# Optimization experiments

Hardware: AMD Instinct MI355X
Metric: run time of the kernel (lower is better)

Reference implementation:

```python
import jax, jax.numpy as jnp
import numpy as np
from jax import lax

B, N, M = 512, 200, 20          # batch, jobs, machines
H1, ME, DI, H2, JD, AH = 128, 32, 128, 256, 256, 256


def setup_inputs() -> dict:
    key = jax.random.key(0)
    ks = jax.random.split(key, 18)
    g = lambda i, s, sc=1.0: jax.random.normal(ks[i], s, jnp.float32) * sc
    return {
        "encoded_jobs": g(0, (B, N, JD)),
        "all_job_processing_times": jax.random.uniform(ks[1], (B, N, M, 2), jnp.float32),
        "num_machines_scalar": jnp.full((B,), float(M), jnp.float32),
        # step1: RNN over machines (input dim 2) + machine-count embedding + FC -> di
        "rnn1_Wih": g(2, (H1, 2), 0.1),
        "rnn1_Whh": g(3, (H1, H1), 0.1),
        "rnn1_b": g(4, (H1,), 0.1),
        "m_w": g(5, (ME,), 0.1),
        "m_b": g(6, (ME,), 0.1),
        "fc_W": g(7, (DI, H1 + ME), 0.1),
        "fc_b": g(8, (DI,), 0.1),
        # step2: single-step RNN cell, initial hidden d0*
        "d0_h": g(9, (1, 1, H2), 0.1),
        "rnn2_Wih": g(10, (H2, DI), 0.1),
        "rnn2_Whh": g(11, (H2, H2), 0.1),
        "rnn2_b": g(12, (H2,), 0.1),
        # additive (Bahdanau) pointer attention
        "att_W1": g(13, (AH, JD), 0.1),
        "att_b1": g(14, (AH,), 0.1),
        "att_W2": g(15, (AH, H2), 0.1),
        "att_b2": g(16, (AH,), 0.1),
        "att_v": g(17, (AH,), 0.1),
    }


def _decode(encoded_jobs, pt, nm, rnn1_Wih, rnn1_Whh, rnn1_b, m_w, m_b,
            fc_W, fc_b, d0_h, rnn2_Wih, rnn2_Whh, rnn2_b,
            att_W1, att_b1, att_W2, att_b2, att_v):
    Bsz, Nn, _ = encoded_jobs.shape
    Mn = pt.shape[2]
    H1d = rnn1_Whh.shape[0]
    H2d = rnn2_Whh.shape[0]
    batch_idx = jnp.arange(Bsz)
    # precompute the job-side attention projection once (same math as per-step)
    pre_att = jnp.einsum('bnd,ad->bna', encoded_jobs, att_W1) + att_b1   # [B,N,AH]
    m_emb = nm[:, None] * m_w[None, :] + m_b                             # [B,ME]

    def step1(P_prev):  # P_prev: [B, M, 2] -> di [B, DI]
        def cell(h, x):
            return jnp.tanh(x @ rnn1_Wih.T + h @ rnn1_Whh.T + rnn1_b), None
        hT, _ = lax.scan(cell, jnp.zeros((Bsz, H1d), P_prev.dtype),
                         jnp.swapaxes(P_prev, 0, 1))
        return jnp.concatenate([hT, m_emb], axis=-1) @ fc_W.T + fc_b

    def decode_step(carry, skey):
        P_prev, h2, avail = carry
        di = step1(P_prev)
        h2n = jnp.tanh(di @ rnn2_Wih.T + h2 @ rnn2_Whh.T + rnn2_b)      # [B,H2]
        q = h2n @ att_W2.T + att_b2                                      # [B,AH]
        scores = jnp.tanh(pre_att + q[:, None, :]) @ att_v               # [B,N]
        masked = jnp.where(avail, scores, -1e9)
        probs = jax.nn.softmax(masked, axis=-1)
        logp = jnp.log(probs + 1e-9)
        chosen = jax.random.categorical(skey, masked)                    # multinomial(probs)
        P_next = pt[batch_idx, chosen]                                   # [B,M,2]
        avail = avail.at[batch_idx, chosen].set(False)
        return (P_next, h2n, avail), (chosen, logp)

    carry0 = (jnp.zeros((Bsz, Mn, 2), encoded_jobs.dtype),
              jnp.broadcast_to(d0_h[0], (Bsz, H2d)),
              jnp.ones((Bsz, Nn), dtype=bool))
    keys = jax.random.split(jax.random.key(42), Nn)  # max_decode_len = N
    _, (idx, logps) = lax.scan(decode_step, carry0, keys)
    return jnp.swapaxes(idx, 0, 1), jnp.swapaxes(logps, 0, 1)  # [B,T], [B,T,N]


def reference(encoded_jobs, all_job_processing_times, num_machines_scalar,
              rnn1_Wih, rnn1_Whh, rnn1_b, m_w, m_b, fc_W, fc_b, d0_h,
              rnn2_Wih, rnn2_Whh, rnn2_b, att_W1, att_b1, att_W2, att_b2, att_v):
    idx, logps = _decode(encoded_jobs, all_job_processing_times, num_machines_scalar,
                         rnn1_Wih, rnn1_Whh, rnn1_b, m_w, m_b, fc_W, fc_b, d0_h,
                         rnn2_Wih, rnn2_Whh, rnn2_b, att_W1, att_b1, att_W2, att_b2, att_v)
    return idx, logps, encoded_jobs
```

## Files before the change

### kernel.cpp

```cpp
#include <hip/hip_runtime.h>
#include <hip/hip_bf16.h>
#include <stdint.h>

#define BB 512
#define NN 200
#define TT 200
#define MM 20
#define H1N 128
#define MEN 32
#define DIN 128
#define H2N 256
#define JDN 256
#define AHN 256

#define PRE_REG 20
#define PRE_LDSB 32

typedef float f4v __attribute__((ext_vector_type(4)));

__device__ __forceinline__ void tf2x32(uint32_t k0, uint32_t k1,
                                       uint32_t x0, uint32_t x1,
                                       uint32_t& o0, uint32_t& o1) {
  uint32_t ks2 = k0 ^ k1 ^ 0x1BD11BDAu;
  x0 += k0; x1 += k1;
#define TF_RND(R) { x0 += x1; x1 = (x1 << (R)) | (x1 >> (32 - (R))); x1 ^= x0; }
  TF_RND(13) TF_RND(15) TF_RND(26) TF_RND(6)   x0 += k1;  x1 += ks2 + 1u;
  TF_RND(17) TF_RND(29) TF_RND(16) TF_RND(24)  x0 += ks2; x1 += k0 + 2u;
  TF_RND(13) TF_RND(15) TF_RND(26) TF_RND(6)   x0 += k0;  x1 += k1 + 3u;
  TF_RND(17) TF_RND(29) TF_RND(16) TF_RND(24)  x0 += k1;  x1 += ks2 + 4u;
  TF_RND(13) TF_RND(15) TF_RND(26) TF_RND(6)   x0 += ks2; x1 += k0 + 5u;
#undef TF_RND
  o0 = x0; o1 = x1;
}

__device__ __forceinline__ float ftanh(float x) {
  float e = __builtin_amdgcn_exp2f(x * 2.8853900817779268f);
  float d = e + 1.0f;
  float r = __builtin_amdgcn_rcpf(d);
  r = r * (2.0f - d * r);
  return 1.0f - 2.0f * r;
}

__global__ void k_transpose(const float* __restrict__ in, float* __restrict__ out,
                            int R, int C) {
  int idx = blockIdx.x * 256 + threadIdx.x;
  if (idx < R * C) { int r = idx / C, c = idx - r * C; out[c * R + r] = in[idx]; }
}

__global__ void k_pack2(const float* __restrict__ w2ih, const float* __restrict__ w2hh,
                        float* __restrict__ Wc2) {
  int idx = blockIdx.x * 256 + threadIdx.x;
  int o = idx & 255, k = idx >> 8;
  Wc2[idx] = (k < 128) ? w2ih[o * 128 + k] : w2hh[o * 256 + (k - 128)];
}

__global__ void k_copy4(const f4v* __restrict__ in, f4v* __restrict__ out, int n4) {
  int i = blockIdx.x * 256 + threadIdx.x;
  if (i < n4) out[i] = in[i];
}

#define NR 20
__global__ __launch_bounds__(256) void k_pre(const float* __restrict__ enc,
                                             const float* __restrict__ W1T,
                                             const float* __restrict__ ab1,
                                             float* __restrict__ pre) {
  const int b = blockIdx.y, n0 = blockIdx.x * NR, tid = threadIdx.x;
  __shared__ __align__(16) float es[NR * JDN];
  for (int r = 0; r < NR; ++r)
    es[r * JDN + tid] = enc[((size_t)(b * NN + n0 + r)) * JDN + tid];
  __syncthreads();
  float acc[NR];
#pragma unroll
  for (int r = 0; r < NR; ++r) acc[r] = 0.0f;
  const f4v* es4 = (const f4v*)es;
  for (int k0 = 0; k0 < JDN; k0 += 4) {
    float w0 = W1T[(k0 + 0) * AHN + tid];
    float w1 = W1T[(k0 + 1) * AHN + tid];
    float w2 = W1T[(k0 + 2) * AHN + tid];
    float w3 = W1T[(k0 + 3) * AHN + tid];
#pragma unroll
    for (int r = 0; r < NR; ++r) {
      f4v e = es4[r * 64 + (k0 >> 2)];
      acc[r] += e.x * w0 + e.y * w1 + e.z * w2 + e.w * w3;
    }
  }
  float bb = ab1[tid];
  for (int r = 0; r < NR; ++r)
    pre[((size_t)(b * NN + n0 + r)) * AHN + tid] = acc[r] + bb;
}

__global__ __launch_bounds__(512) void k_di(
    const float* __restrict__ pt, const float* __restrict__ nm,
    const float* __restrict__ w1ih, const float* __restrict__ b1,
    const float* __restrict__ whh,
    const float* __restrict__ mw, const float* __restrict__ mb,
    const float* __restrict__ fcWT, const float* __restrict__ fcb,
    float* __restrict__ diOut) {
  const int chain = blockIdx.x;
  const int b = chain / 201, n = chain - b * 201;
  const int tid = threadIdx.x;
  const int w = tid >> 6, l = tid & 63;

  __shared__ __align__(16) float hm[320];
  __shared__ float Ps[40];
  __shared__ float partial[512];

  const int j = (w << 4) + (l & 15);
  const int ks = l >> 4;
  float wr[32];
  {
    const float* wp = whh + j * H1N + ks * 32;
#pragma unroll
    for (int i = 0; i < 32; i += 4) {
      f4v t4 = *(const f4v*)(wp + i);
      wr[i] = t4.x; wr[i + 1] = t4.y; wr[i + 2] = t4.z; wr[i + 3] = t4.w;
    }
  }
  const float w1a = w1ih[2 * j], w1b = w1ih[2 * j + 1], b1j = b1[j];
  const float fcb_r = (tid < 128) ? fcb[tid] : 0.0f;

  if (tid < 32)  hm[288 + tid] = nm[b] * mw[tid] + mb[tid];
  if (tid >= 64 && tid < 192) {
    int p = tid - 64;
    hm[(p >> 5) * 36 + (p & 31)] = 0.0f;
  }
  if (tid < 40)
    Ps[tid] = (n < NN) ? pt[((size_t)(b * NN + n)) * (MM * 2) + tid] : 0.0f;
  __syncthreads();

  for (int m = 0; m < MM; ++m) {
    float x0 = Ps[2 * m], x1 = Ps[2 * m + 1];
    float acc = 0.0f;
    const f4v* hm4 = (const f4v*)(hm + (m & 1) * 144 + ks * 36);
#pragma unroll
    for (int i = 0; i < 8; ++i) {
      f4v hv = hm4[i];
      acc += wr[4 * i] * hv.x;     acc += wr[4 * i + 1] * hv.y;
      acc += wr[4 * i + 2] * hv.z; acc += wr[4 * i + 3] * hv.w;
    }
    acc += __shfl_xor(acc, 16);
    acc += __shfl_xor(acc, 32);
    if (ks == 0) {
      float hv = tanhf(acc + x0 * w1a + x1 * w1b + b1j);
      hm[(1 - (m & 1)) * 144 + (j >> 5) * 36 + (j & 31)] = hv;
    }
    __syncthreads();
  }

  {
    const int ksf = tid >> 7, o = tid & 127, k0 = ksf * 40;
    float a0=0,a1=0,a2=0,a3=0,a4=0,a5=0,a6=0,a7=0;
#pragma unroll
    for (int i0 = 0; i0 < 40; i0 += 8) {
#pragma unroll
      for (int q8 = 0; q8 < 8; ++q8) {
        int k = k0 + i0 + q8;
        float hv = (k < 128) ? hm[(k >> 5) * 36 + (k & 31)] : hm[288 + (k - 128)];
        float wv = fcWT[k * 128 + o];
        if (q8 == 0) a0 += hv * wv; else if (q8 == 1) a1 += hv * wv;
        else if (q8 == 2) a2 += hv * wv; else if (q8 == 3) a3 += hv * wv;
        else if (q8 == 4) a4 += hv * wv; else if (q8 == 5) a5 += hv * wv;
        else if (q8 == 6) a6 += hv * wv; else a7 += hv * wv;
      }
    }
    partial[tid] = ((a0 + a1) + (a2 + a3)) + ((a4 + a5) + (a6 + a7));
    __syncthreads();
    if (tid < 128)
      diOut[(size_t)chain * 128 + tid] =
          partial[tid] + partial[128 + tid] + partial[256 + tid] +
          partial[384 + tid] + fcb_r;
  }
}

__global__ __launch_bounds__(512) void k_full(
    const float* __restrict__ pre, const float* __restrict__ attv,
    const float* __restrict__ Wc2, const float* __restrict__ b2,
    const float* __restrict__ attW2T, const float* __restrict__ ab2,
    const float* __restrict__ d0h, const float* __restrict__ di,
    float* __restrict__ out_idx, float* __restrict__ out_logp) {
  const int b0 = blockIdx.x * 2, tid = threadIdx.x;
  const int w = tid >> 6, l = tid & 63;
  const int o = tid & 255, g = tid >> 8;
  const int sg = w >> 2, wg = w & 3;
  const int tid2 = wg * 64 + l;

  __shared__ __align__(16) float wlds[2][8192];
  __shared__ __align__(16) float pre_lds[2][PRE_LDSB * 256];
  __shared__ __align__(16) float xcb[2][2][384];
  __shared__ __align__(16) float qs_g[2][256];
  __shared__ float ms[2][200];
  __shared__ float av[2][200];
  __shared__ float wredv[2][4]; __shared__ int wredi[2][4];
  __shared__ float wmaxs[2][4]; __shared__ float wsums[2][4];
  __shared__ int schosen[2]; __shared__ float smaxs[2], ssums[2];

  float preg[PRE_REG][4];
  const float* pb = pre + (size_t)(b0 + sg) * NN * AHN;
#pragma unroll
  for (int r = 0; r < PRE_REG; ++r) {
    const float* pr = pb + (size_t)(wg * PRE_REG + r) * AHN + l;
#pragma unroll
    for (int jj = 0; jj < 4; ++jj) preg[r][jj] = pr[jj * 64];
  }
  for (int i = tid; i < 2 * PRE_LDSB * 64; i += 512) {
    int bb = i >> 11;
    int rem = i & 2047;
    ((f4v*)pre_lds[bb])[rem] =
        ((const f4v*)(pre + ((size_t)((b0 + bb) * NN + 80)) * AHN))[rem];
  }

  const float b2r  = b2[o];
  const float ab2r = ab2[o];
  const float v0 = attv[l], v1 = attv[l + 64], v2 = attv[l + 128], v3 = attv[l + 192];

  xcb[g][0][128 + o] = d0h[o];
  if (tid < 256) {
    int gg = tid >> 7, k = tid & 127;
    float dv = di[((size_t)((b0 + gg) * 201 + 200)) * 128 + k];
    xcb[gg][0][k] = dv; xcb[gg][1][k] = dv;
  }
  if (tid < 400) { int gg = tid / 200, n = tid - gg * 200; av[gg][n] = 1.0f; }

  {
    const f4v* src = (const f4v*)Wc2;
    f4v* dst = (f4v*)wlds[0];
    dst[tid] = src[tid]; dst[512 + tid] = src[512 + tid];
    dst[1024 + tid] = src[1024 + tid]; dst[1536 + tid] = src[1536 + tid];
  }
  __syncthreads();

  for (int t = 0; t < TT; ++t) {
    const int XB = t & 1, NB = XB ^ 1;
    uint32_t sk0, sk1; tf2x32(0u, 42u, 0u, (uint32_t)t, sk0, sk1);

    float acc1 = 0.0f, acc2 = 0.0f;
    for (int tile = 0; tile < 20; ++tile) {
      const int cur = tile & 1;
      int nt = tile + 1; if (nt == 20) nt = 0;
      const f4v* src = (const f4v*)((nt < 12) ? (Wc2 + nt * 8192)
                                              : (attW2T + (nt - 12) * 8192));
      f4v s0 = src[tid], s1 = src[512 + tid], s2 = src[1024 + tid],
          s3 = src[1536 + tid];

      if (tile == 12) {
        xcb[g][NB][128 + o] = tanhf(acc1 + b2r);
        __syncthreads();
      }

      const float* xsrc = (tile < 12) ? &xcb[g][XB][tile * 32]
                                      : &xcb[g][NB][128 + (tile - 12) * 32];
      f4v xr[8];
#pragma unroll
      for (int i = 0; i < 8; ++i) xr[i] = ((const f4v*)xsrc)[i];

      const float* wl = wlds[cur];
      float a = 0.0f;
#pragma unroll
      for (int kk = 0; kk < 32; ++kk)
        a += xr[kk >> 2][kk & 3] * wl[kk * 256 + o];
      if (tile < 12) acc1 += a; else acc2 += a;

      f4v* wd = (f4v*)wlds[cur ^ 1];
      wd[tid] = s0; wd[512 + tid] = s1; wd[1024 + tid] = s2; wd[1536 + tid] = s3;
      __syncthreads();
    }

    qs_g[g][o] = acc2 + ab2r;
    __syncthreads();

    {
      const float q0 = qs_g[sg][l],       q1 = qs_g[sg][l + 64];
      const float q2 = qs_g[sg][l + 128], q3 = qs_g[sg][l + 192];
#pragma unroll
      for (int r = 0; r < PRE_REG; ++r) {
        float s0 = ftanh(preg[r][0] + q0) * v0;
        float s1 = ftanh(preg[r][1] + q1) * v1;
        float s2 = ftanh(preg[r][2] + q2) * v2;
        float s3 = ftanh(preg[r][3] + q3) * v3;
        float s = (s0 + s1) + (s2 + s3);
#pragma unroll
        for (int d = 32; d > 0; d >>= 1) s += __shfl_down(s, d);
        if (l == 0) ms[sg][wg * PRE_REG + r] = s;
      }
#pragma unroll
      for (int i = 0; i < 8; ++i) {
        const float* pr = pre_lds[sg] + (wg * 8 + i) * 256;
        float s0 = ftanh(pr[l]       + q0) * v0;
        float s1 = ftanh(pr[l + 64]  + q1) * v1;
        float s2 = ftanh(pr[l + 128] + q2) * v2;
        float s3 = ftanh(pr[l + 192] + q3) * v3;
        float s = (s0 + s1) + (s2 + s3);
#pragma unroll
        for (int d = 32; d > 0; d >>= 1) s += __shfl_down(s, d);
        if (l == 0) ms[sg][80 + wg * 8 + i] = s;
      }
      const float* prow = pb + (size_t)(112 + wg * 22) * AHN;
      float c0 = prow[l], c1 = prow[l + 64], c2 = prow[l + 128], c3 = prow[l + 192];
      for (int i = 0; i < 22; ++i) {
        const float* nr = prow + AHN;
        float n0 = 0, n1 = 0, n2 = 0, n3 = 0;
        if (i < 21) { n0 = nr[l]; n1 = nr[l + 64]; n2 = nr[l + 128]; n3 = nr[l + 192]; }
        float s0 = ftanh(c0 + q0) * v0;
        float s1 = ftanh(c1 + q1) * v1;
        float s2 = ftanh(c2 + q2) * v2;
        float s3 = ftanh(c3 + q3) * v3;
        float s = (s0 + s1) + (s2 + s3);
#pragma unroll
        for (int d = 32; d > 0; d >>= 1) s += __shfl_down(s, d);
        if (l == 0) ms[sg][112 + wg * 22 + i] = s;
        c0 = n0; c1 = n1; c2 = n2; c3 = n3; prow = nr;
      }
    }
    __syncthreads();

    float masked = -INFINITY, z = -INFINITY; int zi = 256;
    if (tid2 < NN) {
      masked = (av[sg][tid2] != 0.0f) ? ms[sg][tid2] : -1e9f;
      uint32_t o0, o1; tf2x32(sk0, sk1, 0u, (uint32_t)((b0 + sg) * NN + tid2), o0, o1);
      uint32_t bits = o0 ^ o1;
      float f = __uint_as_float((bits >> 9) | 0x3f800000u) - 1.0f;
      const float TINY = 1.1754943508222875e-38f;
      f = f * (1.0f - TINY) + TINY;
      float gg = -logf(-logf(fmaxf(f, TINY)));
      z = gg + masked;
      zi = tid2;
    }
    {
      float rv = z; int ri = zi; float rm = masked;
#pragma unroll
      for (int d = 32; d > 0; d >>= 1) {
        float ov = __shfl_down(rv, d); int oi = __shfl_down(ri, d);
        float om = __shfl_down(rm, d);
        if (ov > rv || (ov == rv && oi < ri)) { rv = ov; ri = oi; }
        rm = fmaxf(rm, om);
      }
      if (l == 0) { wredv[sg][wg] = rv; wredi[sg][wg] = ri; wmaxs[sg][wg] = rm; }
    }
    __syncthreads();
    if (tid2 == 0) {
      float bv = wredv[sg][0]; int bi = wredi[sg][0]; float bm = wmaxs[sg][0];
#pragma unroll
      for (int k = 1; k < 4; ++k) {
        float ov = wredv[sg][k]; int oi = wredi[sg][k];
        if (ov > bv || (ov == bv && oi < bi)) { bv = ov; bi = oi; }
        bm = fmaxf(bm, wmaxs[sg][k]);
      }
      schosen[sg] = bi; smaxs[sg] = bm;
    }
    __syncthreads();
    const int chosen = schosen[sg]; const float maxm = smaxs[sg];
    if (tid2 < 128) {
      float dv = di[((size_t)((b0 + sg) * 201 + chosen)) * 128 + tid2];
      xcb[sg][0][tid2] = dv; xcb[sg][1][tid2] = dv;
    }
    if (tid2 == chosen) av[sg][tid2] = 0.0f;
    float ev = (tid2 < NN) ? expf(masked - maxm) : 0.0f;
    {
      float sv = ev;
#pragma unroll
      for (int d = 32; d > 0; d >>= 1) sv += __shfl_down(sv, d);
      if (l == 0) wsums[sg][wg] = sv;
    }
    __syncthreads();
    if (tid2 == 0)
      ssums[sg] = (wsums[sg][0] + wsums[sg][1]) + (wsums[sg][2] + wsums[sg][3]);
    __syncthreads();
    if (tid2 < NN)
      out_logp[((size_t)((b0 + sg) * TT + t)) * NN + tid2] =
          logf(ev / ssums[sg] + 1e-9f);
    if (tid2 == 0) out_idx[(b0 + sg) * TT + t] = (float)chosen;
    __syncthreads();
  }
}

extern "C" void kernel_launch(void* const* d_in, const int* in_sizes, int n_in,
                              void* d_out, int out_size, void* d_ws, size_t ws_size,
                              hipStream_t stream) {
  const float* enc  = (const float*)d_in[0];
  const float* pt   = (const float*)d_in[1];
  const float* nm   = (const float*)d_in[2];
  const float* w1ih = (const float*)d_in[3];
  const float* whh1 = (const float*)d_in[4];
  const float* b1   = (const float*)d_in[5];
  const float* mw   = (const float*)d_in[6];
  const float* mb   = (const float*)d_in[7];
  const float* fcW  = (const float*)d_in[8];
  const float* fcb  = (const float*)d_in[9];
  const float* d0h  = (const float*)d_in[10];
  const float* w2ih = (const float*)d_in[11];
  const float* w2hh = (const float*)d_in[12];
  const float* b2   = (const float*)d_in[13];
  const float* aw1  = (const float*)d_in[14];
  const float* ab1  = (const float*)d_in[15];
  const float* aw2  = (const float*)d_in[16];
  const float* ab2  = (const float*)d_in[17];
  const float* av   = (const float*)d_in[18];

  float* out      = (float*)d_out;
  float* out_idx  = out;
  float* out_logp = out + 102400;
  float* out_enc  = out + 102400 + 20480000;
  float* pre      = out_enc;

  float* ws     = (float*)d_ws;
  float* W1T    = ws;
  float* fcWT   = ws + 65536;
  float* attW2T = ws + 86016;
  float* Wc2    = ws + 151552;
  float* di     = ws + 249856;

  k_transpose<<<(65536 + 255) / 256, 256, 0, stream>>>(aw1, W1T,    256, 256);
  k_transpose<<<(20480 + 255) / 256, 256, 0, stream>>>(fcW, fcWT,   128, 160);
  k_transpose<<<(65536 + 255) / 256, 256, 0, stream>>>(aw2, attW2T, 256, 256);
  k_pack2<<<384, 256, 0, stream>>>(w2ih, w2hh, Wc2);

  dim3 gpre(NN / NR, BB);
  k_pre<<<gpre, 256, 0, stream>>>(enc, W1T, ab1, pre);

  k_di<<<BB * 201, 512, 0, stream>>>(pt, nm, w1ih, b1, whh1, mw, mb, fcWT, fcb, di);

  k_full<<<BB / 2, 512, 0, stream>>>(pre, av, Wc2, b2, attW2T, ab2, d0h, di,
                                     out_idx, out_logp);

  k_copy4<<<(6553600 + 255) / 256, 256, 0, stream>>>((const f4v*)enc,
                                                     (f4v*)out_enc, 6553600);
}
```

Before: 9.153 ms.

## Split matvec K across halves for weight reuse; pair attention row reductions

Each 256-thread half now processes half of each 32-wide K tile for both batch rows, so every LDS weight load is reused for two rows. The halves' partial sums are combined through a new shared partial buffer, which adds extra barriers. The attention score loops now process two rows per wave and merge their cross-lane reductions with an xor-32 shuffle, cutting shuffle count per row.

```diff
diff --git a/kernel.cpp b/kernel.cpp
--- a/kernel.cpp
+++ b/kernel.cpp
@@ -180,13 +180,14 @@
     float* __restrict__ out_idx, float* __restrict__ out_logp) {
   const int b0 = blockIdx.x * 2, tid = threadIdx.x;
   const int w = tid >> 6, l = tid & 63;
-  const int o = tid & 255, g = tid >> 8;
+  const int o = tid & 255, hh = tid >> 8;
   const int sg = w >> 2, wg = w & 3;
   const int tid2 = wg * 64 + l;
 
   __shared__ __align__(16) float wlds[2][8192];
   __shared__ __align__(16) float pre_lds[2][PRE_LDSB * 256];
   __shared__ __align__(16) float xcb[2][2][384];
+  __shared__ __align__(16) float partial[1024];
   __shared__ __align__(16) float qs_g[2][256];
   __shared__ float ms[2][200];
   __shared__ float av[2][200];
@@ -213,7 +214,7 @@
   const float ab2r = ab2[o];
   const float v0 = attv[l], v1 = attv[l + 64], v2 = attv[l + 128], v3 = attv[l + 192];
 
-  xcb[g][0][128 + o] = d0h[o];
+  xcb[hh][0][128 + o] = d0h[o];
   if (tid < 256) {
     int gg = tid >> 7, k = tid & 127;
     float dv = di[((size_t)((b0 + gg) * 201 + 200)) * 128 + k];
@@ -233,7 +234,7 @@
     const int XB = t & 1, NB = XB ^ 1;
     uint32_t sk0, sk1; tf2x32(0u, 42u, 0u, (uint32_t)t, sk0, sk1);
 
-    float acc1 = 0.0f, acc2 = 0.0f;
+    float a1A = 0.0f, a1B = 0.0f, a2A = 0.0f, a2B = 0.0f;
     for (int tile = 0; tile < 20; ++tile) {
       const int cur = tile & 1;
       int nt = tile + 1; if (nt == 20) nt = 0;
@@ -243,72 +244,114 @@
           s3 = src[1536 + tid];
 
       if (tile == 12) {
-        xcb[g][NB][128 + o] = tanhf(acc1 + b2r);
+        partial[(hh * 2 + 0) * 256 + o] = a1A;
+        partial[(hh * 2 + 1) * 256 + o] = a1B;
         __syncthreads();
-      }
-
-      const float* xsrc = (tile < 12) ? &xcb[g][XB][tile * 32]
-                                      : &xcb[g][NB][128 + (tile - 12) * 32];
-      f4v xr[8];
-#pragma unroll
-      for (int i = 0; i < 8; ++i) xr[i] = ((const f4v*)xsrc)[i];
-
-      const float* wl = wlds[cur];
-      float a = 0.0f;
-#pragma unroll
-      for (int kk = 0; kk < 32; ++kk)
-        a += xr[kk >> 2][kk & 3] * wl[kk * 256 + o];
-      if (tile < 12) acc1 += a; else acc2 += a;
+        xcb[hh][NB][128 + o] =
+            tanhf(partial[(0 * 2 + hh) * 256 + o] +
+                  partial[(1 * 2 + hh) * 256 + o] + b2r);
+        __syncthreads();
+      }
+
+      const int koff = (tile < 12) ? (tile * 32 + hh * 16)
+                                   : (128 + (tile - 12) * 32 + hh * 16);
+      const int bufsel = (tile < 12) ? XB : NB;
+      const int xbase = (tile < 12) ? koff : (128 + koff - 128);
+      const f4v* xA4 = (const f4v*)(&xcb[0][bufsel][koff]);
+      const f4v* xB4 = (const f4v*)(&xcb[1][bufsel][koff]);
+      f4v xa0 = xA4[0], xa1 = xA4[1], xa2 = xA4[2], xa3 = xA4[3];
+      f4v xb0 = xB4[0], xb1 = xB4[1], xb2 = xB4[2], xb3 = xB4[3];
+      (void)xbase;
+
+      const float* wl = wlds[cur] + (size_t)(hh * 16) * 256 + o;
+      float aA = 0.0f, aB = 0.0f;
+#pragma unroll
+      for (int kk = 0; kk < 16; ++kk) {
+        float wv = wl[kk * 256];
+        float xav = (kk < 4) ? xa0[kk] : (kk < 8) ? xa1[kk - 4]
+                   : (kk < 12) ? xa2[kk - 8] : xa3[kk - 12];
+        float xbv = (kk < 4) ? xb0[kk] : (kk < 8) ? xb1[kk - 4]
+                   : (kk < 12) ? xb2[kk - 8] : xb3[kk - 12];
+        aA += xav * wv;
+        aB += xbv * wv;
+      }
+      if (tile < 12) { a1A += aA; a1B += aB; } else { a2A += aA; a2B += aB; }
 
       f4v* wd = (f4v*)wlds[cur ^ 1];
       wd[tid] = s0; wd[512 + tid] = s1; wd[1024 + tid] = s2; wd[1536 + tid] = s3;
       __syncthreads();
     }
 
-    qs_g[g][o] = acc2 + ab2r;
+    partial[(hh * 2 + 0) * 256 + o] = a2A;
+    partial[(hh * 2 + 1) * 256 + o] = a2B;
+    __syncthreads();
+    qs_g[hh][o] = partial[(0 * 2 + hh) * 256 + o] +
+                  partial[(1 * 2 + hh) * 256 + o] + ab2r;
     __syncthreads();
 
     {
       const float q0 = qs_g[sg][l],       q1 = qs_g[sg][l + 64];
       const float q2 = qs_g[sg][l + 128], q3 = qs_g[sg][l + 192];
-#pragma unroll
-      for (int r = 0; r < PRE_REG; ++r) {
-        float s0 = ftanh(preg[r][0] + q0) * v0;
-        float s1 = ftanh(preg[r][1] + q1) * v1;
-        float s2 = ftanh(preg[r][2] + q2) * v2;
-        float s3 = ftanh(preg[r][3] + q3) * v3;
-        float s = (s0 + s1) + (s2 + s3);
-#pragma unroll
-        for (int d = 32; d > 0; d >>= 1) s += __shfl_down(s, d);
-        if (l == 0) ms[sg][wg * PRE_REG + r] = s;
-      }
-#pragma unroll
-      for (int i = 0; i < 8; ++i) {
-        const float* pr = pre_lds[sg] + (wg * 8 + i) * 256;
-        float s0 = ftanh(pr[l]       + q0) * v0;
-        float s1 = ftanh(pr[l + 64]  + q1) * v1;
-        float s2 = ftanh(pr[l + 128] + q2) * v2;
-        float s3 = ftanh(pr[l + 192] + q3) * v3;
-        float s = (s0 + s1) + (s2 + s3);
-#pragma unroll
-        for (int d = 32; d > 0; d >>= 1) s += __shfl_down(s, d);
-        if (l == 0) ms[sg][80 + wg * 8 + i] = s;
+
+#pragma unroll
+      for (int r = 0; r < PRE_REG; r += 2) {
+        float sA = (ftanh(preg[r][0] + q0) * v0 + ftanh(preg[r][1] + q1) * v1) +
+                   (ftanh(preg[r][2] + q2) * v2 + ftanh(preg[r][3] + q3) * v3);
+        float sB = (ftanh(preg[r+1][0] + q0) * v0 + ftanh(preg[r+1][1] + q1) * v1) +
+                   (ftanh(preg[r+1][2] + q2) * v2 + ftanh(preg[r+1][3] + q3) * v3);
+        float p = (l < 32) ? sA : sB;
+        float q_ = (l < 32) ? sB : sA;
+        float tt = p + __shfl_xor(q_, 32);
+        tt += __shfl_down(tt, 16); tt += __shfl_down(tt, 8);
+        tt += __shfl_down(tt, 4);  tt += __shfl_down(tt, 2);
+        tt += __shfl_down(tt, 1);
+        if (l == 0)  ms[sg][wg * PRE_REG + r]     = tt;
+        if (l == 32) ms[sg][wg * PRE_REG + r + 1] = tt;
+      }
+#pragma unroll
+      for (int i = 0; i < 8; i += 2) {
+        const float* prA = pre_lds[sg] + (wg * 8 + i) * 256;
+        const float* prB = prA + 256;
+        float sA = (ftanh(prA[l] + q0) * v0 + ftanh(prA[l + 64] + q1) * v1) +
+                   (ftanh(prA[l + 128] + q2) * v2 + ftanh(prA[l + 192] + q3) * v3);
+        float sB = (ftanh(prB[l] + q0) * v0 + ftanh(prB[l + 64] + q1) * v1) +
+                   (ftanh(prB[l + 128] + q2) * v2 + ftanh(prB[l + 192] + q3) * v3);
+        float p = (l < 32) ? sA : sB;
+        float q_ = (l < 32) ? sB : sA;
+        float tt = p + __shfl_xor(q_, 32);
+        tt += __shfl_down(tt, 16); tt += __shfl_down(tt, 8);
+        tt += __shfl_down(tt, 4);  tt += __shfl_down(tt, 2);
+        tt += __shfl_down(tt, 1);
+        if (l == 0)  ms[sg][80 + wg * 8 + i]     = tt;
+        if (l == 32) ms[sg][80 + wg * 8 + i + 1] = tt;
       }
       const float* prow = pb + (size_t)(112 + wg * 22) * AHN;
-      float c0 = prow[l], c1 = prow[l + 64], c2 = prow[l + 128], c3 = prow[l + 192];
-      for (int i = 0; i < 22; ++i) {
-        const float* nr = prow + AHN;
-        float n0 = 0, n1 = 0, n2 = 0, n3 = 0;
-        if (i < 21) { n0 = nr[l]; n1 = nr[l + 64]; n2 = nr[l + 128]; n3 = nr[l + 192]; }
-        float s0 = ftanh(c0 + q0) * v0;
-        float s1 = ftanh(c1 + q1) * v1;
-        float s2 = ftanh(c2 + q2) * v2;
-        float s3 = ftanh(c3 + q3) * v3;
-        float s = (s0 + s1) + (s2 + s3);
-#pragma unroll
-        for (int d = 32; d > 0; d >>= 1) s += __shfl_down(s, d);
-        if (l == 0) ms[sg][112 + wg * 22 + i] = s;
-        c0 = n0; c1 = n1; c2 = n2; c3 = n3; prow = nr;
+      float cA0 = prow[l], cA1 = prow[l + 64], cA2 = prow[l + 128], cA3 = prow[l + 192];
+      float cB0 = prow[AHN + l], cB1 = prow[AHN + l + 64],
+            cB2 = prow[AHN + l + 128], cB3 = prow[AHN + l + 192];
+      for (int pi = 0; pi < 11; ++pi) {
+        const float* nx = prow + 2 * AHN;
+        float nA0 = 0, nA1 = 0, nA2 = 0, nA3 = 0, nB0 = 0, nB1 = 0, nB2 = 0, nB3 = 0;
+        if (pi < 10) {
+          nA0 = nx[l]; nA1 = nx[l + 64]; nA2 = nx[l + 128]; nA3 = nx[l + 192];
+          nB0 = nx[AHN + l]; nB1 = nx[AHN + l + 64];
+          nB2 = nx[AHN + l + 128]; nB3 = nx[AHN + l + 192];
+        }
+        float sA = (ftanh(cA0 + q0) * v0 + ftanh(cA1 + q1) * v1) +
+                   (ftanh(cA2 + q2) * v2 + ftanh(cA3 + q3) * v3);
+        float sB = (ftanh(cB0 + q0) * v0 + ftanh(cB1 + q1) * v1) +
+                   (ftanh(cB2 + q2) * v2 + ftanh(cB3 + q3) * v3);
+        float p = (l < 32) ? sA : sB;
+        float q_ = (l < 32) ? sB : sA;
+        float tt = p + __shfl_xor(q_, 32);
+        tt += __shfl_down(tt, 16); tt += __shfl_down(tt, 8);
+        tt += __shfl_down(tt, 4);  tt += __shfl_down(tt, 2);
+        tt += __shfl_down(tt, 1);
+        if (l == 0)  ms[sg][112 + wg * 22 + 2 * pi]     = tt;
+        if (l == 32) ms[sg][112 + wg * 22 + 2 * pi + 1] = tt;
+        cA0 = nA0; cA1 = nA1; cA2 = nA2; cA3 = nA3;
+        cB0 = nB0; cB1 = nB1; cB2 = nB2; cB3 = nB3;
+        prow = nx;
       }
     }
     __syncthreads();
```

After: 16.72 ms. +82.6%, slower.

## Split K across thread halves so each weight LDS read serves both batch rows

Applied to the files above, without the earlier changes.

The per-step GEMV over the weight tiles is repartitioned. Previously each half of the block computed one batch row over the full 32-row tile. Now each half takes 16 of the K rows and computes both batch rows, so every weight value read from LDS is used twice. Partial sums are combined through a new shared buffer, which costs extra syncthreads and LDS traffic at the tanh point and after the loop.

```diff
diff --git a/kernel.cpp b/kernel.cpp
--- a/kernel.cpp
+++ b/kernel.cpp
@@ -180,13 +180,14 @@
     float* __restrict__ out_idx, float* __restrict__ out_logp) {
   const int b0 = blockIdx.x * 2, tid = threadIdx.x;
   const int w = tid >> 6, l = tid & 63;
-  const int o = tid & 255, g = tid >> 8;
+  const int o = tid & 255, hh = tid >> 8;
   const int sg = w >> 2, wg = w & 3;
   const int tid2 = wg * 64 + l;
 
   __shared__ __align__(16) float wlds[2][8192];
   __shared__ __align__(16) float pre_lds[2][PRE_LDSB * 256];
   __shared__ __align__(16) float xcb[2][2][384];
+  __shared__ __align__(16) float partial[1024];
   __shared__ __align__(16) float qs_g[2][256];
   __shared__ float ms[2][200];
   __shared__ float av[2][200];
@@ -213,7 +214,7 @@
   const float ab2r = ab2[o];
   const float v0 = attv[l], v1 = attv[l + 64], v2 = attv[l + 128], v3 = attv[l + 192];
 
-  xcb[g][0][128 + o] = d0h[o];
+  xcb[hh][0][128 + o] = d0h[o];
   if (tid < 256) {
     int gg = tid >> 7, k = tid & 127;
     float dv = di[((size_t)((b0 + gg) * 201 + 200)) * 128 + k];
@@ -233,7 +234,7 @@
     const int XB = t & 1, NB = XB ^ 1;
     uint32_t sk0, sk1; tf2x32(0u, 42u, 0u, (uint32_t)t, sk0, sk1);
 
-    float acc1 = 0.0f, acc2 = 0.0f;
+    float a1A = 0.0f, a1B = 0.0f, a2A = 0.0f, a2B = 0.0f;
     for (int tile = 0; tile < 20; ++tile) {
       const int cur = tile & 1;
       int nt = tile + 1; if (nt == 20) nt = 0;
@@ -243,29 +244,47 @@
           s3 = src[1536 + tid];
 
       if (tile == 12) {
-        xcb[g][NB][128 + o] = tanhf(acc1 + b2r);
+        partial[(hh * 2 + 0) * 256 + o] = a1A;
+        partial[(hh * 2 + 1) * 256 + o] = a1B;
         __syncthreads();
-      }
-
-      const float* xsrc = (tile < 12) ? &xcb[g][XB][tile * 32]
-                                      : &xcb[g][NB][128 + (tile - 12) * 32];
-      f4v xr[8];
-#pragma unroll
-      for (int i = 0; i < 8; ++i) xr[i] = ((const f4v*)xsrc)[i];
-
-      const float* wl = wlds[cur];
-      float a = 0.0f;
-#pragma unroll
-      for (int kk = 0; kk < 32; ++kk)
-        a += xr[kk >> 2][kk & 3] * wl[kk * 256 + o];
-      if (tile < 12) acc1 += a; else acc2 += a;
+        xcb[hh][NB][128 + o] =
+            tanhf(partial[(0 * 2 + hh) * 256 + o] +
+                  partial[(1 * 2 + hh) * 256 + o] + b2r);
+        __syncthreads();
+      }
+
+      const int koff = (tile < 12) ? (tile * 32 + hh * 16)
+                                   : (128 + (tile - 12) * 32 + hh * 16);
+      const int bufsel = (tile < 12) ? XB : NB;
+      const f4v* xA4 = (const f4v*)(&xcb[0][bufsel][koff]);
+      const f4v* xB4 = (const f4v*)(&xcb[1][bufsel][koff]);
+      f4v xa0 = xA4[0], xa1 = xA4[1], xa2 = xA4[2], xa3 = xA4[3];
+      f4v xb0 = xB4[0], xb1 = xB4[1], xb2 = xB4[2], xb3 = xB4[3];
+
+      const float* wl = wlds[cur] + (size_t)(hh * 16) * 256 + o;
+      float aA = 0.0f, aB = 0.0f;
+#pragma unroll
+      for (int kk = 0; kk < 16; ++kk) {
+        float wv = wl[kk * 256];
+        float xav = (kk < 4) ? xa0[kk] : (kk < 8) ? xa1[kk - 4]
+                   : (kk < 12) ? xa2[kk - 8] : xa3[kk - 12];
+        float xbv = (kk < 4) ? xb0[kk] : (kk < 8) ? xb1[kk - 4]
+                   : (kk < 12) ? xb2[kk - 8] : xb3[kk - 12];
+        aA += xav * wv;
+        aB += xbv * wv;
+      }
+      if (tile < 12) { a1A += aA; a1B += aB; } else { a2A += aA; a2B += aB; }
 
       f4v* wd = (f4v*)wlds[cur ^ 1];
       wd[tid] = s0; wd[512 + tid] = s1; wd[1024 + tid] = s2; wd[1536 + tid] = s3;
       __syncthreads();
     }
 
-    qs_g[g][o] = acc2 + ab2r;
+    partial[(hh * 2 + 0) * 256 + o] = a2A;
+    partial[(hh * 2 + 1) * 256 + o] = a2B;
+    __syncthreads();
+    qs_g[hh][o] = partial[(0 * 2 + hh) * 256 + o] +
+                  partial[(1 * 2 + hh) * 256 + o] + ab2r;
     __syncthreads();
 
     {
```

After: 18.81 ms. 106% more time.
